# Kernel optimization log

Measured on AMD Instinct MI355X. Metric: run time of the kernel, lower is better.

Reference implementation:

```python
import jax, jax.numpy as jnp
import numpy as np

E = 2.718281828459045  # math.e
B, A, N = 128, 512, 256


def setup_inputs() -> dict:
    key = jax.random.key(0)
    k1, k2, k3 = jax.random.split(key, 3)
    # atomic numbers: positive integers (1..89) stored as float32
    atomic_numbers = jax.random.randint(k1, (B, A), 1, 90).astype(jnp.float32)
    # neighbor indices into the atom axis [0, A)
    neighbors = jax.random.randint(k2, (B, A, N), 0, A).astype(jnp.int32)
    # pairwise distances, positive
    r_ij = jax.random.uniform(k3, (B, A, N), dtype=jnp.float32) * 5.0 + 0.5
    return {"atomic_numbers": atomic_numbers, "neighbors": neighbors, "r_ij": r_ij}


def reference(atomic_numbers, neighbors, r_ij):
    # a_i: [B, A, 1] central-atom atomic numbers
    a_i = atomic_numbers[:, :, None]
    # gather neighbor atomic numbers: out[b,i,j] = atomic_numbers[b, neighbors[b,i,j]]
    a_j = jax.vmap(lambda an, nb: an[nb])(atomic_numbers, neighbors)  # [B, A, N]
    # fused elementwise edit: exp(-0.05*e * (a_i*a_j)^1.01 / (a_i+a_j)^1.1)
    dist_edit = jnp.exp(-0.05 * E * jnp.power(a_i * a_j, 1.01)
                        / jnp.power(a_i + a_j, 1.1))
    return r_ij + dist_edit
```

## Files before the change

### kernel.cpp

```cpp
#include <hip/hip_runtime.h>


#define BB 128
#define AA 512
#define NN 256
#define ROWS 32
#define TPB 256
#define TABN 8192

typedef int   v4i __attribute__((ext_vector_type(4)));
typedef float v4f __attribute__((ext_vector_type(4)));

__device__ __forceinline__ float tab_entry(int idx) {
    int zi = idx / 90, zj = idx - zi * 90;
    float p = fmaxf((float)(zi * zj), 1.0f);
    float s = fmaxf((float)(zi + zj), 1.0f);
    const float c = -0.05f * 2.718281828459045f;
    return __expf(c * __powf(p, 1.01f) / __powf(s, 1.1f));
}

__global__ void RAN_72567767433723_build_tab(_Float16* __restrict__ tabg) {
    int idx = blockIdx.x * blockDim.x + threadIdx.x;
    tabg[idx] = (_Float16)tab_entry(idx);
}

template <bool LOAD_TAB>
__global__ __launch_bounds__(TPB, 4) void RAN_72567767433723_kernel(
    const float* __restrict__ an,
    const int*   __restrict__ nbrs,
    const float* __restrict__ rij,
    float*       __restrict__ out,
    const _Float16* __restrict__ tabg)
{
    __shared__ _Float16       tab[TABN];
    __shared__ unsigned short zz[AA];

    const int tid      = threadIdx.x;
    const int b        = blockIdx.x >> 4;
    const int row_base = (blockIdx.x & 15) * ROWS;

    if (LOAD_TAB) {
        #pragma unroll
        for (int i = 0; i < TABN * 2 / (16 * TPB); ++i) {
            int k = i * TPB + tid;
            ((v4i*)tab)[k] = ((const v4i*)tabg)[k];
        }
    } else {
        for (int idx = tid; idx < TABN; idx += TPB)
            tab[idx] = (_Float16)tab_entry(idx);
    }
    #pragma unroll
    for (int i = tid; i < AA; i += TPB)
        zz[i] = (unsigned short)(int)(an[b * AA + i] + 0.5f);
    __syncthreads();

    const int w  = tid >> 6;
    const int l  = tid & 63;
    const int a0 = row_base + w;
    const size_t base = ((size_t)(b * AA + a0)) * NN + (size_t)(l * 4);

    v4i nb[8]; v4f rj[8];
    #pragma unroll
    for (int it = 0; it < 8; ++it) {
        const size_t e = base + (size_t)(it * 4) * NN;
        nb[it] = __builtin_nontemporal_load((const v4i*)(nbrs + e));
        rj[it] = __builtin_nontemporal_load((const v4f*)(rij + e));
    }

    int tb[8];
    #pragma unroll
    for (int it = 0; it < 8; ++it)
        tb[it] = (int)zz[a0 + it * 4] * 90;

    #pragma unroll
    for (int it = 0; it < 8; ++it) {
        const size_t e = base + (size_t)(it * 4) * NN;
        v4f o;
        o.x = rj[it].x + (float)tab[tb[it] + (int)zz[nb[it].x]];
        o.y = rj[it].y + (float)tab[tb[it] + (int)zz[nb[it].y]];
        o.z = rj[it].z + (float)tab[tb[it] + (int)zz[nb[it].z]];
        o.w = rj[it].w + (float)tab[tb[it] + (int)zz[nb[it].w]];
        __builtin_nontemporal_store(o, (v4f*)(out + e));
    }
}

extern "C" void kernel_launch(void* const* d_in, const int* in_sizes, int n_in,
                              void* d_out, int out_size, void* d_ws, size_t ws_size,
                              hipStream_t stream) {
    const float* an  = (const float*)d_in[0];
    const int*   nbr = (const int*)d_in[1];
    const float* rij = (const float*)d_in[2];
    float*       o   = (float*)d_out;

    const int grid = (BB * AA) / ROWS;

    if (ws_size >= (size_t)TABN * sizeof(_Float16)) {
        _Float16* tabg = (_Float16*)d_ws;
        RAN_72567767433723_build_tab<<<TABN / TPB, TPB, 0, stream>>>(tabg);
        RAN_72567767433723_kernel<true><<<grid, TPB, 0, stream>>>(an, nbr, rij, o, tabg);
    } else {
        RAN_72567767433723_kernel<false><<<grid, TPB, 0, stream>>>(an, nbr, rij, o, nullptr);
    }
}
```

Baseline: 165.1 us.

## Double-buffer neighbor loads and process 64 rows per block

```diff
diff --git a/kernel.cpp b/kernel.cpp
--- a/kernel.cpp
+++ b/kernel.cpp
@@ -4,7 +4,7 @@
 #define BB 128
 #define AA 512
 #define NN 256
-#define ROWS 32
+#define ROWS 64
 #define TPB 256
 #define TABN 8192
 
@@ -36,8 +36,8 @@
     __shared__ unsigned short zz[AA];
 
     const int tid      = threadIdx.x;
-    const int b        = blockIdx.x >> 4;
-    const int row_base = (blockIdx.x & 15) * ROWS;
+    const int b        = blockIdx.x >> 3;
+    const int row_base = (blockIdx.x & 7) * ROWS;
 
     if (LOAD_TAB) {
         #pragma unroll
@@ -59,28 +59,43 @@
     const int a0 = row_base + w;
     const size_t base = ((size_t)(b * AA + a0)) * NN + (size_t)(l * 4);
 
-    v4i nb[8]; v4f rj[8];
+    v4i nb[2][4]; v4f rj[2][4];
+
     #pragma unroll
-    for (int it = 0; it < 8; ++it) {
-        const size_t e = base + (size_t)(it * 4) * NN;
-        nb[it] = __builtin_nontemporal_load((const v4i*)(nbrs + e));
-        rj[it] = __builtin_nontemporal_load((const v4f*)(rij + e));
+    for (int j = 0; j < 4; ++j) {
+        const size_t e0 = base + (size_t)(j * 4) * NN;
+        const size_t e1 = base + (size_t)((4 + j) * 4) * NN;
+        nb[0][j] = *(const v4i*)(nbrs + e0);
+        rj[0][j] = *(const v4f*)(rij + e0);
+        nb[1][j] = *(const v4i*)(nbrs + e1);
+        rj[1][j] = *(const v4f*)(rij + e1);
     }
 
-    int tb[8];
     #pragma unroll
-    for (int it = 0; it < 8; ++it)
-        tb[it] = (int)zz[a0 + it * 4] * 90;
+    for (int c = 0; c < 4; ++c) {
+        const int buf = c & 1;
 
-    #pragma unroll
-    for (int it = 0; it < 8; ++it) {
-        const size_t e = base + (size_t)(it * 4) * NN;
-        v4f o;
-        o.x = rj[it].x + (float)tab[tb[it] + (int)zz[nb[it].x]];
-        o.y = rj[it].y + (float)tab[tb[it] + (int)zz[nb[it].y]];
-        o.z = rj[it].z + (float)tab[tb[it] + (int)zz[nb[it].z]];
-        o.w = rj[it].w + (float)tab[tb[it] + (int)zz[nb[it].w]];
-        __builtin_nontemporal_store(o, (v4f*)(out + e));
+        #pragma unroll
+        for (int j = 0; j < 4; ++j) {
+            const int it = c * 4 + j;
+            const int tb = (int)zz[a0 + it * 4] * 90;
+            const size_t e = base + (size_t)(it * 4) * NN;
+            v4f o;
+            o.x = rj[buf][j].x + (float)tab[tb + (int)zz[nb[buf][j].x]];
+            o.y = rj[buf][j].y + (float)tab[tb + (int)zz[nb[buf][j].y]];
+            o.z = rj[buf][j].z + (float)tab[tb + (int)zz[nb[buf][j].z]];
+            o.w = rj[buf][j].w + (float)tab[tb + (int)zz[nb[buf][j].w]];
+            __builtin_nontemporal_store(o, (v4f*)(out + e));
+        }
+
+        if (c < 2) {
+            #pragma unroll
+            for (int j = 0; j < 4; ++j) {
+                const size_t e = base + (size_t)(((c + 2) * 4 + j) * 4) * NN;
+                nb[buf][j] = *(const v4i*)(nbrs + e);
+                rj[buf][j] = *(const v4f*)(rij + e);
+            }
+        }
     }
 }
 
```

Result: slower. 180.0 us (+9.0%).
